# Kernel tuning notes

Hardware: AMD Instinct MI355X
Metric: run time of the kernel (lower is better)

Reference implementation:

```python
import jax, jax.numpy as jnp
import numpy as np

N = 8192
D = 200


def setup_inputs() -> dict:
    key = jax.random.key(0)
    k1, k2, k3 = jax.random.split(key, 3)
    G_p = jax.random.normal(k1, (N, D), dtype=jnp.float32)
    # scale weights so exp(b + e) stays in a sane numeric range
    wb = jax.random.normal(k2, (D, 1), dtype=jnp.float32) * 0.02
    we = jax.random.normal(k3, (D, 1), dtype=jnp.float32) * 0.02
    return {"G_p": G_p, "wb": wb, "we": we, "k": 100}


def reference(G_p, wb, we, k):
    # begin / end scores: [N, 1]
    b_P = G_p @ wb
    e_P = G_p @ we
    # outer-sum span scores -> [N, N]
    numerator = jnp.exp(b_P + e_P.T)
    denominator = jnp.sum(numerator)
    candidate_probs = numerator / denominator
    upper = jnp.triu(candidate_probs)
    flat = upper.reshape(-1)
    k_max_values, flat_idx = jax.lax.top_k(flat, k)
    W = upper.shape[1]
    orig_indices = jnp.stack([flat_idx // W, flat_idx % W], axis=1)
    return orig_indices, k_max_values
```

## Files before the change

kernel.cpp:

```cpp
#include <hip/hip_runtime.h>
#include <math.h>

#define NN 8192
#define DD 200
#define KK 100

#define NBINS 1024
#define HSCALE 64.0f
#define BINW 0.015625f
#define CAND_CAP 4096
#define ROW_CAP 1024
#define COL_CAP 1024

#define OFF_B 0
#define OFF_E 8192
#define OFF_PB 16384
#define OFF_PE 18432

__global__ __launch_bounds__(256) void k_be(const float* __restrict__ G,
                                            const float* __restrict__ wb,
                                            const float* __restrict__ we,
                                            float* __restrict__ wsf) {
    __shared__ float seb[4], see[4];
    int gid = blockIdx.x * 256 + threadIdx.x;
    int row = gid >> 6;
    int lane = gid & 63;
    int wave = threadIdx.x >> 6;
    float pb = 0.f, pe = 0.f;
    if (lane < 50) {
        float4 g = ((const float4*)(G + (size_t)row * DD))[lane];
        float4 B = ((const float4*)wb)[lane];
        float4 E = ((const float4*)we)[lane];
        pb = fmaf(g.x, B.x, fmaf(g.y, B.y, fmaf(g.z, B.z, g.w * B.w)));
        pe = fmaf(g.x, E.x, fmaf(g.y, E.y, fmaf(g.z, E.z, g.w * E.w)));
    }
    for (int off = 32; off; off >>= 1) {
        pb += __shfl_xor(pb, off, 64);
        pe += __shfl_xor(pe, off, 64);
    }
    if (lane == 0) {
        wsf[OFF_B + row] = pb;
        wsf[OFF_E + row] = pe;
        seb[wave] = expf(pb);
        see[wave] = expf(pe);
    }
    __syncthreads();
    if (threadIdx.x == 0) {
        wsf[OFF_PB + blockIdx.x] = (seb[0] + seb[1]) + (seb[2] + seb[3]);
        wsf[OFF_PE + blockIdx.x] = (see[0] + see[1]) + (see[2] + see[3]);
    }
}

__device__ __forceinline__ unsigned ford(float f) {
    unsigned u = __float_as_uint(f);
    return u ^ ((u & 0x80000000u) ? 0xFFFFFFFFu : 0x80000000u);
}

__global__ __launch_bounds__(1024) void k_tail(const float* __restrict__ wsf,
                                               float* __restrict__ out) {
    __shared__ unsigned long long kv[CAND_CAP];
    __shared__ unsigned hb_par[2][NBINS];
    __shared__ unsigned he_par[2][NBINS];
    __shared__ unsigned sfx[NBINS];
    __shared__ int      rows_s[ROW_CAP];
    __shared__ float    rowb_s[ROW_CAP];
    __shared__ int      cols_s[COL_CAP];
    __shared__ float    cole_s[COL_CAP];
    __shared__ float    fr_sb[16], fr_se[16];
    __shared__ int      fr_eb[16], fr_bb[16];
    __shared__ unsigned wred[32], wtail_s[16];
    __shared__ unsigned nrows_s, ncols_s, ncand_s;
    __shared__ int      lo_s;
    __shared__ float    sums_s[4];

    int tid = threadIdx.x, wave = tid >> 6, lane = tid & 63;
    int par = wave & 1;

    hb_par[0][tid] = 0u; hb_par[1][tid] = 0u;
    he_par[0][tid] = 0u; he_par[1][tid] = 0u;
    if (tid == 0) { nrows_s = 0u; ncols_s = 0u; ncand_s = 0u; lo_s = 0; }
    __syncthreads();

    float4 bv0 = ((const float4*)(wsf + OFF_B))[tid];
    float4 ev0 = ((const float4*)(wsf + OFF_E))[tid];
    float4 bv1 = ((const float4*)(wsf + OFF_B))[tid + 1024];
    float4 ev1 = ((const float4*)(wsf + OFF_E))[tid + 1024];
    {
        int p;
        p = (int)fmaf(bv0.x, HSCALE, 512.f); atomicAdd(&hb_par[par][min(max(p,0),NBINS-1)], 1u);
        p = (int)fmaf(bv0.y, HSCALE, 512.f); atomicAdd(&hb_par[par][min(max(p,0),NBINS-1)], 1u);
        p = (int)fmaf(bv0.z, HSCALE, 512.f); atomicAdd(&hb_par[par][min(max(p,0),NBINS-1)], 1u);
        p = (int)fmaf(bv0.w, HSCALE, 512.f); atomicAdd(&hb_par[par][min(max(p,0),NBINS-1)], 1u);
        p = (int)fmaf(bv1.x, HSCALE, 512.f); atomicAdd(&hb_par[par][min(max(p,0),NBINS-1)], 1u);
        p = (int)fmaf(bv1.y, HSCALE, 512.f); atomicAdd(&hb_par[par][min(max(p,0),NBINS-1)], 1u);
        p = (int)fmaf(bv1.z, HSCALE, 512.f); atomicAdd(&hb_par[par][min(max(p,0),NBINS-1)], 1u);
        p = (int)fmaf(bv1.w, HSCALE, 512.f); atomicAdd(&hb_par[par][min(max(p,0),NBINS-1)], 1u);
        p = (int)fmaf(ev0.x, HSCALE, 512.f); atomicAdd(&he_par[par][min(max(p,0),NBINS-1)], 1u);
        p = (int)fmaf(ev0.y, HSCALE, 512.f); atomicAdd(&he_par[par][min(max(p,0),NBINS-1)], 1u);
        p = (int)fmaf(ev0.z, HSCALE, 512.f); atomicAdd(&he_par[par][min(max(p,0),NBINS-1)], 1u);
        p = (int)fmaf(ev0.w, HSCALE, 512.f); atomicAdd(&he_par[par][min(max(p,0),NBINS-1)], 1u);
        p = (int)fmaf(ev1.x, HSCALE, 512.f); atomicAdd(&he_par[par][min(max(p,0),NBINS-1)], 1u);
        p = (int)fmaf(ev1.y, HSCALE, 512.f); atomicAdd(&he_par[par][min(max(p,0),NBINS-1)], 1u);
        p = (int)fmaf(ev1.z, HSCALE, 512.f); atomicAdd(&he_par[par][min(max(p,0),NBINS-1)], 1u);
        p = (int)fmaf(ev1.w, HSCALE, 512.f); atomicAdd(&he_par[par][min(max(p,0),NBINS-1)], 1u);
    }

    float psb = wsf[OFF_PB + tid] + wsf[OFF_PB + 1024 + tid];
    float pse = wsf[OFF_PE + tid] + wsf[OFF_PE + 1024 + tid];
    for (int off = 32; off; off >>= 1) {
        psb += __shfl_xor(psb, off, 64);
        pse += __shfl_xor(pse, off, 64);
    }
    if (lane == 0) { fr_sb[wave] = psb; fr_se[wave] = pse; }
    __syncthreads();

    unsigned hb = hb_par[0][tid] + hb_par[1][tid];
    unsigned he = he_par[0][tid] + he_par[1][tid];
    hb_par[0][tid] = hb;
    int ebin = (he != 0u) ? tid : -1;
    int bbin = (hb != 0u) ? tid : -1;
    for (int off = 32; off; off >>= 1) {
        ebin = max(ebin, __shfl_xor(ebin, off, 64));
        bbin = max(bbin, __shfl_xor(bbin, off, 64));
    }
    if (lane == 0) { fr_eb[wave] = ebin; fr_bb[wave] = bbin; }
    unsigned v = he;
    for (int off = 1; off < 64; off <<= 1) {
        unsigned t = __shfl_down(v, off, 64);
        if (lane + off < 64) v += t;
    }
    if (lane == 0) wtail_s[wave] = v;
    __syncthreads();
    if (tid == 0) {
        float a = 0.f, b = 0.f; int c = -1, d = -1;
        for (int i = 0; i < 16; ++i) {
            a += fr_sb[i]; b += fr_se[i];
            c = max(c, fr_eb[i]); d = max(d, fr_bb[i]);
        }
        sums_s[0] = a; sums_s[1] = b;
        sums_s[2] = -8.0f + (float)(c + 1) * BINW;
        sums_s[3] = -8.0f + (float)(d + 1) * BINW;
        unsigned acc = 0, tails[16];
        for (int w = 15; w >= 0; --w) { tails[w] = acc; acc += wtail_s[w]; }
        for (int w = 0; w < 16; ++w) wtail_s[w] = tails[w];
    }
    __syncthreads();
    sfx[tid] = v + wtail_s[wave];
    __syncthreads();

    const unsigned TARGET = 2u * KK;
    int half = lane >> 5, l5 = lane & 31;
    int chunk = 32;
    for (int round = 0; round < 2; ++round) {
        int t = lo_s + (2 * wave + half + 1) * chunk;
        unsigned c = 0;
        for (int k = 0; k < 32; ++k) {
            int p = l5 + (k << 5);
            int idx = t + 512 - p;
            unsigned sv = (idx <= 0) ? sfx[0] : ((idx > NBINS - 1) ? 0u : sfx[idx]);
            c += hb_par[0][p] * sv;
        }
        for (int off = 16; off; off >>= 1) c += __shfl_xor(c, off, 64);
        if (l5 == 0) wred[2 * wave + half] = c;
        __syncthreads();
        if (tid == 0) {
            for (int w = 31; w >= 0; --w)
                if (wred[w] >= TARGET) { lo_s += (w + 1) * chunk; break; }
        }
        __syncthreads();
        chunk >>= 5;
    }
    float thr = -8.0f + (float)(lo_s - 1) * BINW;
    float emax = sums_s[2], bmax = sums_s[3];

#define CANDB(val, row)                                                    \
    if ((val) + emax >= thr) {                                             \
        unsigned pos = atomicAdd(&nrows_s, 1u);                            \
        if (pos < ROW_CAP) { rows_s[pos] = (row); rowb_s[pos] = (val); }   \
    }
#define CANDE(val, row)                                                    \
    if ((val) + bmax >= thr) {                                             \
        unsigned pos = atomicAdd(&ncols_s, 1u);                            \
        if (pos < COL_CAP) { cols_s[pos] = (row); cole_s[pos] = (val); }   \
    }
    {
        int r0 = 4 * tid, r1 = 4 * (tid + 1024);
        CANDB(bv0.x, r0 + 0) CANDB(bv0.y, r0 + 1) CANDB(bv0.z, r0 + 2) CANDB(bv0.w, r0 + 3)
        CANDB(bv1.x, r1 + 0) CANDB(bv1.y, r1 + 1) CANDB(bv1.z, r1 + 2) CANDB(bv1.w, r1 + 3)
        CANDE(ev0.x, r0 + 0) CANDE(ev0.y, r0 + 1) CANDE(ev0.z, r0 + 2) CANDE(ev0.w, r0 + 3)
        CANDE(ev1.x, r1 + 0) CANDE(ev1.y, r1 + 1) CANDE(ev1.z, r1 + 2) CANDE(ev1.w, r1 + 3)
    }
    __syncthreads();
    int nr = (int)min(nrows_s, (unsigned)ROW_CAP);
    int nc = (int)min(ncols_s, (unsigned)COL_CAP);

    int tot = nr * nc;
    for (int idx = tid; idx < tot; idx += 1024) {
        int ri = idx / nc, cj = idx - ri * nc;
        int r = rows_s[ri], j = cols_s[cj];
        if (j < r) continue;
        float s = rowb_s[ri] + cole_s[cj];
        if (s >= thr) {
            unsigned pos = atomicAdd(&ncand_s, 1u);
            if (pos < CAND_CAP) {
                unsigned fi = ((unsigned)r << 13) | (unsigned)j;
                kv[pos] = ((unsigned long long)ford(s) << 32) | (unsigned)(~fi);
            }
        }
    }
    __syncthreads();

    unsigned M = min(ncand_s, (unsigned)CAND_CAP);
    float inv_den = 1.0f / (sums_s[0] * sums_s[1]);
    for (unsigned c2 = tid; c2 < M; c2 += 1024) {
        unsigned long long kk = kv[c2];
        int rank = 0;
        for (unsigned m = 0; m < M; ++m) rank += (kv[m] > kk);
        if (rank < KK) {
            unsigned hi = (unsigned)(kk >> 32);
            unsigned fi = ~(unsigned)kk;
            unsigned u = (hi & 0x80000000u) ? (hi ^ 0x80000000u) : ~hi;
            float vv = __uint_as_float(u);
            out[2 * rank]     = (float)(fi >> 13);
            out[2 * rank + 1] = (float)(fi & 8191u);
            out[200 + rank]   = expf(vv) * inv_den;
        }
    }
}

extern "C" void kernel_launch(void* const* d_in, const int* in_sizes, int n_in,
                              void* d_out, int out_size, void* d_ws, size_t ws_size,
                              hipStream_t stream) {
    const float* G  = (const float*)d_in[0];
    const float* wb = (const float*)d_in[1];
    const float* we = (const float*)d_in[2];
    float* out = (float*)d_out;
    float* wsf = (float*)d_ws;

    hipLaunchKernelGGL(k_be, dim3(2048), dim3(256), 0, stream, G, wb, we, wsf);
    hipLaunchKernelGGL(k_tail, dim3(1), dim3(1024), 0, stream, wsf, out);
}
```

Measured before the change: 77.67 us.

## Replace single-thread reductions with wave-level shuffles and ballots in tail kernel

```diff
diff --git a/kernel.cpp b/kernel.cpp
--- a/kernel.cpp
+++ b/kernel.cpp
@@ -59,8 +59,8 @@
 __global__ __launch_bounds__(1024) void k_tail(const float* __restrict__ wsf,
                                                float* __restrict__ out) {
     __shared__ unsigned long long kv[CAND_CAP];
-    __shared__ unsigned hb_par[2][NBINS];
-    __shared__ unsigned he_par[2][NBINS];
+    __shared__ unsigned hb_par[4][NBINS];
+    __shared__ unsigned he_par[4][NBINS];
     __shared__ unsigned sfx[NBINS];
     __shared__ int      rows_s[ROW_CAP];
     __shared__ float    rowb_s[ROW_CAP];
@@ -68,23 +68,24 @@
     __shared__ float    cole_s[COL_CAP];
     __shared__ float    fr_sb[16], fr_se[16];
     __shared__ int      fr_eb[16], fr_bb[16];
-    __shared__ unsigned wred[32], wtail_s[16];
+    __shared__ unsigned wtail_s[16];
+    __shared__ unsigned wred[32], wred2[32];
     __shared__ unsigned nrows_s, ncols_s, ncand_s;
-    __shared__ int      lo_s;
-    __shared__ float    sums_s[4];
 
     int tid = threadIdx.x, wave = tid >> 6, lane = tid & 63;
-    int par = wave & 1;
-
-    hb_par[0][tid] = 0u; hb_par[1][tid] = 0u;
-    he_par[0][tid] = 0u; he_par[1][tid] = 0u;
-    if (tid == 0) { nrows_s = 0u; ncols_s = 0u; ncand_s = 0u; lo_s = 0; }
+    int par = wave & 3;
+
+    hb_par[0][tid] = 0u; hb_par[1][tid] = 0u; hb_par[2][tid] = 0u; hb_par[3][tid] = 0u;
+    he_par[0][tid] = 0u; he_par[1][tid] = 0u; he_par[2][tid] = 0u; he_par[3][tid] = 0u;
+    if (tid == 0) { nrows_s = 0u; ncols_s = 0u; ncand_s = 0u; }
     __syncthreads();
 
     float4 bv0 = ((const float4*)(wsf + OFF_B))[tid];
     float4 ev0 = ((const float4*)(wsf + OFF_E))[tid];
     float4 bv1 = ((const float4*)(wsf + OFF_B))[tid + 1024];
     float4 ev1 = ((const float4*)(wsf + OFF_E))[tid + 1024];
+    float p0 = wsf[OFF_PB + tid], p1 = wsf[OFF_PB + 1024 + tid];
+    float q0 = wsf[OFF_PE + tid], q1 = wsf[OFF_PE + 1024 + tid];
     {
         int p;
         p = (int)fmaf(bv0.x, HSCALE, 512.f); atomicAdd(&hb_par[par][min(max(p,0),NBINS-1)], 1u);
@@ -104,9 +105,7 @@
         p = (int)fmaf(ev1.z, HSCALE, 512.f); atomicAdd(&he_par[par][min(max(p,0),NBINS-1)], 1u);
         p = (int)fmaf(ev1.w, HSCALE, 512.f); atomicAdd(&he_par[par][min(max(p,0),NBINS-1)], 1u);
     }
-
-    float psb = wsf[OFF_PB + tid] + wsf[OFF_PB + 1024 + tid];
-    float pse = wsf[OFF_PE + tid] + wsf[OFF_PE + 1024 + tid];
+    float psb = p0 + p1, pse = q0 + q1;
     for (int off = 32; off; off >>= 1) {
         psb += __shfl_xor(psb, off, 64);
         pse += __shfl_xor(pse, off, 64);
@@ -114,8 +113,8 @@
     if (lane == 0) { fr_sb[wave] = psb; fr_se[wave] = pse; }
     __syncthreads();
 
-    unsigned hb = hb_par[0][tid] + hb_par[1][tid];
-    unsigned he = he_par[0][tid] + he_par[1][tid];
+    unsigned hb = hb_par[0][tid] + hb_par[1][tid] + hb_par[2][tid] + hb_par[3][tid];
+    unsigned he = he_par[0][tid] + he_par[1][tid] + he_par[2][tid] + he_par[3][tid];
     hb_par[0][tid] = hb;
     int ebin = (he != 0u) ? tid : -1;
     int bbin = (hb != 0u) ? tid : -1;
@@ -131,28 +130,30 @@
     }
     if (lane == 0) wtail_s[wave] = v;
     __syncthreads();
-    if (tid == 0) {
-        float a = 0.f, b = 0.f; int c = -1, d = -1;
-        for (int i = 0; i < 16; ++i) {
-            a += fr_sb[i]; b += fr_se[i];
-            c = max(c, fr_eb[i]); d = max(d, fr_bb[i]);
-        }
-        sums_s[0] = a; sums_s[1] = b;
-        sums_s[2] = -8.0f + (float)(c + 1) * BINW;
-        sums_s[3] = -8.0f + (float)(d + 1) * BINW;
-        unsigned acc = 0, tails[16];
-        for (int w = 15; w >= 0; --w) { tails[w] = acc; acc += wtail_s[w]; }
-        for (int w = 0; w < 16; ++w) wtail_s[w] = tails[w];
-    }
-    __syncthreads();
-    sfx[tid] = v + wtail_s[wave];
+
+    int w16 = lane & 15;
+    float sb = fr_sb[w16], se = fr_se[w16];
+    int eb = fr_eb[w16], bb = fr_bb[w16];
+    unsigned wt = wtail_s[w16];
+    if (w16 <= wave) wt = 0u;
+    for (int off = 8; off; off >>= 1) {
+        sb += __shfl_xor(sb, off, 64);
+        se += __shfl_xor(se, off, 64);
+        eb = max(eb, __shfl_xor(eb, off, 64));
+        bb = max(bb, __shfl_xor(bb, off, 64));
+        wt += __shfl_xor(wt, off, 64);
+    }
+    sfx[tid] = v + wt;
+    float emax = -8.0f + (float)(eb + 1) * BINW;
+    float bmax = -8.0f + (float)(bb + 1) * BINW;
+    float inv_den = 1.0f / (sb * se);
     __syncthreads();
 
     const unsigned TARGET = 2u * KK;
     int half = lane >> 5, l5 = lane & 31;
-    int chunk = 32;
-    for (int round = 0; round < 2; ++round) {
-        int t = lo_s + (2 * wave + half + 1) * chunk;
+    int lo = 0;
+    {
+        int t = (2 * wave + half + 1) * 32;
         unsigned c = 0;
         for (int k = 0; k < 32; ++k) {
             int p = l5 + (k << 5);
@@ -162,16 +163,34 @@
         }
         for (int off = 16; off; off >>= 1) c += __shfl_xor(c, off, 64);
         if (l5 == 0) wred[2 * wave + half] = c;
-        __syncthreads();
-        if (tid == 0) {
-            for (int w = 31; w >= 0; --w)
-                if (wred[w] >= TARGET) { lo_s += (w + 1) * chunk; break; }
-        }
-        __syncthreads();
-        chunk >>= 5;
-    }
-    float thr = -8.0f + (float)(lo_s - 1) * BINW;
-    float emax = sums_s[2], bmax = sums_s[3];
+    }
+    __syncthreads();
+    {
+        unsigned cc = wred[lane & 31];
+        unsigned long long mk = __ballot(cc >= TARGET);
+        unsigned m32 = (unsigned)(mk & 0xFFFFFFFFull);
+        if (m32) lo += (32 - __builtin_clz(m32)) * 32;
+    }
+    {
+        int t = lo + (2 * wave + half + 1);
+        unsigned c = 0;
+        for (int k = 0; k < 32; ++k) {
+            int p = l5 + (k << 5);
+            int idx = t + 512 - p;
+            unsigned sv = (idx <= 0) ? sfx[0] : ((idx > NBINS - 1) ? 0u : sfx[idx]);
+            c += hb_par[0][p] * sv;
+        }
+        for (int off = 16; off; off >>= 1) c += __shfl_xor(c, off, 64);
+        if (l5 == 0) wred2[2 * wave + half] = c;
+    }
+    __syncthreads();
+    {
+        unsigned cc = wred2[lane & 31];
+        unsigned long long mk = __ballot(cc >= TARGET);
+        unsigned m32 = (unsigned)(mk & 0xFFFFFFFFull);
+        if (m32) lo += (32 - __builtin_clz(m32));
+    }
+    float thr = -8.0f + (float)(lo - 1) * BINW;
 
 #define CANDB(val, row)                                                    \
     if ((val) + emax >= thr) {                                             \
@@ -211,7 +230,6 @@
     __syncthreads();
 
     unsigned M = min(ncand_s, (unsigned)CAND_CAP);
-    float inv_den = 1.0f / (sums_s[0] * sums_s[1]);
     for (unsigned c2 = tid; c2 < M; c2 += 1024) {
         unsigned long long kk = kv[c2];
         int rank = 0;
```

Measured after the change: 75.33 us. 3.0% less time.
